# Kernel optimization log

Hardware: AMD Instinct MI355X
Metric: run time of the kernel (lower is better)

## Reference

```python
import jax, jax.numpy as jnp
import numpy as np

B, N, CIN, COUT = 4, 4096, 64, 64

def setup_inputs() -> dict:
    key = jax.random.key(0)
    k1, k2, k3, k4, k5 = jax.random.split(key, 5)
    X = jax.random.normal(k1, (B, N, CIN), dtype=jnp.float32)
    A = jax.random.uniform(k2, (N, N), dtype=jnp.float32)
    weight1 = jax.random.normal(k3, (CIN, COUT), dtype=jnp.float32) * 0.05
    weight2 = jax.random.normal(k4, (1 * COUT, COUT), dtype=jnp.float32) * 0.05
    alpha = jax.random.normal(k5, (2 * COUT, 1), dtype=jnp.float32) * 0.05
    return {"X": X, "A": A, "weight1": weight1, "weight2": weight2, "alpha": alpha}

def reference(X, A, weight1, weight2, alpha):
    n = A.shape[0]
    c = weight1.shape[1]
    b = X.shape[0]
    # add self loops on the adjacency diagonal
    idx = jnp.arange(n)
    adj = A.at[idx, idx].set(1.0)
    # node transform: [B,N,C]
    out = jnp.matmul(X, weight1)
    # edge feature (P=1): [N,N,1], row-normalized over j (axis=1)
    E = adj[:, :, None]
    E_wave = E / E.sum(axis=1, keepdims=True)
    # attention scores via rank-1 decomposition of alpha
    att_l = jnp.matmul(out, alpha[:c])   # [B,N,1]
    att_r = jnp.matmul(out, alpha[c:])   # [B,N,1]
    scores = jax.nn.leaky_relu(att_l @ jnp.swapaxes(att_r, 1, 2))  # [B,N,N]
    # exp + edge-feature weighting: [P,B,N,N]
    att = jnp.einsum('bij,ijp->pbij', jnp.exp(scores), E_wave)
    # manual softmax-style normalization over neighbors j
    att = att / att.sum(axis=-1, keepdims=True)
    # aggregate: [B,N,P,C] -> [B,N,P*C]
    agg = jnp.einsum('pbij,bjc->bipc', att, out).reshape(b, n, -1)
    return jnp.matmul(agg, weight2)
```

## Files before the change

### kernel.cpp

```cpp
#include <hip/hip_runtime.h>
#include <hip/hip_bf16.h>

typedef __attribute__((ext_vector_type(8))) short short8;
typedef __attribute__((ext_vector_type(4))) float floatx4;
typedef unsigned int u32;

#define NN 4096

static __device__ __forceinline__ unsigned f2bf_rne(float x) {
    union { float f; unsigned u; } v; v.f = x;
    unsigned r = v.u + 0x7fffu + ((v.u >> 16) & 1u);
    return r >> 16;
}
static __device__ __forceinline__ float bf2f(unsigned hi) {
    union { unsigned u; float f; } v; v.u = hi << 16; return v.f;
}

static __device__ __forceinline__ void gld16(void* l, const void* g) {
    __builtin_amdgcn_global_load_lds(
        (const __attribute__((address_space(1))) u32*)g,
        (__attribute__((address_space(3))) u32*)l, 16, 0, 0);
}

__global__ __launch_bounds__(256, 1)
void wc_kernel(const float* __restrict__ W1,
               const float* __restrict__ W2,
               const float* __restrict__ alpha,
               float* __restrict__ WcstG,
               float* __restrict__ w1aG) {
    __shared__ __align__(16) float W1s[64 * 68];
    __shared__ __align__(16) float W2s[64 * 68];
    __shared__ float als[128];
    const int t = threadIdx.x;
    #pragma unroll
    for (int s = 0; s < 4; ++s) {
        int idx = s * 1024 + t * 4;
        int r = idx >> 6, cc = idx & 63;
        *(float4*)&W1s[r * 68 + cc] = *(const float4*)(W1 + idx);
        *(float4*)&W2s[r * 68 + cc] = *(const float4*)(W2 + idx);
    }
    if (t < 128) als[t] = alpha[t];
    __syncthreads();
    const int k = t >> 2, nq = t & 3;
    float acc[16];
    #pragma unroll
    for (int i = 0; i < 16; ++i) acc[i] = 0.f;
    for (int mm = 0; mm < 64; ++mm) {
        float w1v = W1s[k * 68 + mm];
        #pragma unroll
        for (int i = 0; i < 16; ++i)
            acc[i] += w1v * W2s[mm * 68 + nq * 16 + i];
    }
    #pragma unroll
    for (int i = 0; i < 16; ++i)
        WcstG[(nq * 16 + i) * 68 + k] = acc[i];
    if (t < 64) {
        float sl = 0.f, sr = 0.f;
        for (int cc2 = 0; cc2 < 64; ++cc2) {
            float wv = W1s[t * 68 + cc2];
            sl += wv * als[cc2];
            sr += wv * als[64 + cc2];
        }
        w1aG[t] = sl; w1aG[64 + t] = sr;
    }
}

__global__ __launch_bounds__(256, 4)
void prep_kernel(const float* __restrict__ X,
                 const float* __restrict__ WcstG,
                 const float* __restrict__ w1aG,
                 unsigned short* __restrict__ Gt,
                 float* __restrict__ lv,
                 float* __restrict__ rv) {
    __shared__ __align__(16) char sm[17920];
    float* Wcst = (float*)sm;
    float* w1s  = (float*)(sm + 17408);
    float* GsT  = (float*)sm;

    const int t = threadIdx.x;
    const int row0 = blockIdx.x * 64;
    const int b = row0 >> 12, n0 = row0 & (NN - 1);
    const int w = t >> 6, lane = t & 63;
    const int m = lane & 15, q = lane >> 4;

    const int row = row0 + w * 16 + m;
    const float* xp = X + (size_t)row * 64;
    float4 x0 = *(const float4*)(xp + q * 8);
    float4 x1 = *(const float4*)(xp + q * 8 + 4);
    float4 x2 = *(const float4*)(xp + 32 + q * 8);
    float4 x3 = *(const float4*)(xp + 32 + q * 8 + 4);

    #pragma unroll
    for (int it = 0; it < 5; ++it) {
        int i = it * 1024 + t * 4;
        if (i < 4352) *(float4*)&Wcst[i] = *(const float4*)(WcstG + i);
    }
    if (t < 128) w1s[t] = w1aG[t];
    __syncthreads();

    const float xs[16] = {x0.x,x0.y,x0.z,x0.w, x1.x,x1.y,x1.z,x1.w,
                          x2.x,x2.y,x2.z,x2.w, x3.x,x3.y,x3.z,x3.w};

    float pl = 0.f, pr = 0.f;
    #pragma unroll
    for (int ks = 0; ks < 2; ++ks)
        #pragma unroll
        for (int j = 0; j < 8; ++j) {
            int k = ks * 32 + q * 8 + j;
            float xv = xs[ks * 8 + j];
            pl += xv * w1s[k];
            pr += xv * w1s[64 + k];
        }
    pl += __shfl_xor(pl, 16, 64); pl += __shfl_xor(pl, 32, 64);
    pr += __shfl_xor(pr, 16, 64); pr += __shfl_xor(pr, 32, 64);
    if (q == 0) { lv[row] = pl; rv[row] = pr; }

    short8 ah[2], al[2];
    #pragma unroll
    for (int ks = 0; ks < 2; ++ks)
        #pragma unroll
        for (int j = 0; j < 8; ++j) {
            float f = xs[ks * 8 + j];
            unsigned hb = f2bf_rne(f);
            float res = f - bf2f(hb);
            ah[ks][j] = (short)hb;
            al[ks][j] = (short)f2bf_rne(res);
        }

    short8 bfr[4][2];
    #pragma unroll
    for (int nt = 0; nt < 4; ++nt)
        #pragma unroll
        for (int ks = 0; ks < 2; ++ks) {
            const float* wp = &Wcst[(nt * 16 + m) * 68 + ks * 32 + q * 8];
            float4 w0 = *(const float4*)wp;
            float4 w1 = *(const float4*)(wp + 4);
            short8 bf;
            bf[0] = (short)f2bf_rne(w0.x); bf[1] = (short)f2bf_rne(w0.y);
            bf[2] = (short)f2bf_rne(w0.z); bf[3] = (short)f2bf_rne(w0.w);
            bf[4] = (short)f2bf_rne(w1.x); bf[5] = (short)f2bf_rne(w1.y);
            bf[6] = (short)f2bf_rne(w1.z); bf[7] = (short)f2bf_rne(w1.w);
            bfr[nt][ks] = bf;
        }

    floatx4 acc[4] = {{0,0,0,0},{0,0,0,0},{0,0,0,0},{0,0,0,0}};
    #pragma unroll
    for (int ks = 0; ks < 2; ++ks)
        #pragma unroll
        for (int nt = 0; nt < 4; ++nt) {
            acc[nt] = __builtin_amdgcn_mfma_f32_16x16x32_bf16(ah[ks], bfr[nt][ks], acc[nt], 0, 0, 0);
            acc[nt] = __builtin_amdgcn_mfma_f32_16x16x32_bf16(al[ks], bfr[nt][ks], acc[nt], 0, 0, 0);
        }

    __syncthreads();
    #pragma unroll
    for (int nt = 0; nt < 4; ++nt)
        #pragma unroll
        for (int rg = 0; rg < 4; ++rg)
            GsT[(nt * 16 + m) * 68 + w * 16 + q * 4 + rg] = acc[nt][rg];
    __syncthreads();
    unsigned* Gu = (unsigned*)Gt;
    #pragma unroll
    for (int it2 = 0; it2 < 8; ++it2) {
        int c2 = (t >> 5) + it2 * 8;
        int np = t & 31;
        unsigned lo = f2bf_rne(GsT[c2 * 68 + 2 * np]);
        unsigned hi = f2bf_rne(GsT[c2 * 68 + 2 * np + 1]);
        Gu[(((((size_t)(b * 64 + c2)) << 12) + n0) >> 1) + np] = lo | (hi << 16);
    }
}

__global__ __launch_bounds__(1024, 4)
void attn_kernel(const float* __restrict__ A,
                 const unsigned short* __restrict__ Gt,
                 const float* __restrict__ lv,
                 const float* __restrict__ rv,
                 float* __restrict__ out) {
    __shared__ __align__(16) char sm[65536];

    const int bx = blockIdx.x;
    const int i0 = (bx & 63) * 64;
    const int b  = bx >> 6;
    const int t = threadIdx.x;
    const int wave = t >> 6, lane = t & 63;
    const int grp = wave >> 2, wsub = wave & 3;
    const int m = lane & 15, q = lane >> 4;
    const int irow = wsub * 16 + m;

    const float* aRow = A + (size_t)(i0 + irow) * NN + grp * 1024 + q * 8;
    const unsigned short* gRow = Gt + (((size_t)(b * 64 + irow)) << 12) + grp * 1024 + q * 8;
    const float* rvg = rv + (size_t)b * NN + grp * 1024 + q * 8;
    char* gdst = sm + grp * 4096 + wsub * 1024;

    const float li = lv[b * NN + i0 + irow] * 1.44269504f;
    const float li001 = li * 0.01f;

    gld16(gdst, gRow);
    float4 a0 = *(const float4*)(aRow);
    float4 a1 = *(const float4*)(aRow + 4);
    float4 r0 = *(const float4*)(rvg);
    float4 r1 = *(const float4*)(rvg + 4);

    const bool diag_grp = ((i0 >> 10) == grp);
    const int jd = (i0 + irow) - grp * 1024;

    floatx4 acc0 = {0,0,0,0}, acc1 = {0,0,0,0}, acc2 = {0,0,0,0}, acc3 = {0,0,0,0};
    float dsum = 0.f;

    unsigned short* Gbuf = (unsigned short*)sm;

    #pragma unroll 4
    for (int cc = 0; cc < 32; ++cc) {
        if (cc < 31) gld16(gdst + ((cc + 1) & 3) * 16384, gRow + (cc + 1) * 32);

        float aa[8] = {a0.x, a0.y, a0.z, a0.w, a1.x, a1.y, a1.z, a1.w};
        if (diag_grp && ((jd >> 5) == cc)) {
            const int dd = jd - (cc * 32 + q * 8);
            #pragma unroll
            for (int e = 0; e < 8; ++e) if (dd == e) aa[e] = 1.0f;
        }
        const float rr[8] = {r0.x, r0.y, r0.z, r0.w, r1.x, r1.y, r1.z, r1.w};
        unsigned up[8];
        #pragma unroll
        for (int e = 0; e < 8; ++e) {
            float s = fmaxf(li * rr[e], li001 * rr[e]);
            float ev = __builtin_amdgcn_exp2f(s) * aa[e];
            unsigned u = __float_as_uint(ev) + 0x8000u;
            up[e] = u;
            dsum += __uint_as_float(u & 0xffff0000u);
        }
        union { unsigned u[4]; short8 s8; } cv;
        cv.u[0] = __builtin_amdgcn_perm(up[1], up[0], 0x07060302u);
        cv.u[1] = __builtin_amdgcn_perm(up[3], up[2], 0x07060302u);
        cv.u[2] = __builtin_amdgcn_perm(up[5], up[4], 0x07060302u);
        cv.u[3] = __builtin_amdgcn_perm(up[7], up[6], 0x07060302u);
        const short8 afr = cv.s8;

        { const int jn = (cc < 31) ? (cc + 1) * 32 : 0;
          a0 = *(const float4*)(aRow + jn);
          a1 = *(const float4*)(aRow + jn + 4);
          r0 = *(const float4*)(rvg + jn);
          r1 = *(const float4*)(rvg + jn + 4); }

        __syncthreads();
        {
            const unsigned short* Gb = Gbuf + (cc & 3) * 8192 + grp * 2048;
            const short8 b0 = *(const short8*)&Gb[lane * 8];
            const short8 b1 = *(const short8*)&Gb[512 + lane * 8];
            const short8 b2 = *(const short8*)&Gb[1024 + lane * 8];
            const short8 b3 = *(const short8*)&Gb[1536 + lane * 8];
            acc0 = __builtin_amdgcn_mfma_f32_16x16x32_bf16(afr, b0, acc0, 0, 0, 0);
            acc1 = __builtin_amdgcn_mfma_f32_16x16x32_bf16(afr, b1, acc1, 0, 0, 0);
            acc2 = __builtin_amdgcn_mfma_f32_16x16x32_bf16(afr, b2, acc2, 0, 0, 0);
            acc3 = __builtin_amdgcn_mfma_f32_16x16x32_bf16(afr, b3, acc3, 0, 0, 0);
        }
    }

    dsum += __shfl_xor(dsum, 16, 64);
    dsum += __shfl_xor(dsum, 32, 64);

    __syncthreads();
    float* red = (float*)sm;
    const int il = t >> 4, c4 = t & 15;
    float4 osum = {0.f, 0.f, 0.f, 0.f};
    float dtot = 0.f;
    #pragma unroll
    for (int pass = 0; pass < 2; ++pass) {
        if ((grp >> 1) == pass) {
            float* rp_ = red + (grp & 1) * 4352;
            #pragma unroll
            for (int nt = 0; nt < 4; ++nt) {
                floatx4 av = nt == 0 ? acc0 : nt == 1 ? acc1 : nt == 2 ? acc2 : acc3;
                #pragma unroll
                for (int rg = 0; rg < 4; ++rg)
                    rp_[(wsub * 16 + q * 4 + rg) * 68 + nt * 16 + m] = av[rg];
            }
            if (q == 0) rp_[(wsub * 16 + m) * 68 + 64] = dsum;
        }
        __syncthreads();
        {
            float4 v0 = *(const float4*)&red[il * 68 + c4 * 4];
            float4 v1 = *(const float4*)&red[4352 + il * 68 + c4 * 4];
            osum.x += v0.x + v1.x; osum.y += v0.y + v1.y;
            osum.z += v0.z + v1.z; osum.w += v0.w + v1.w;
            dtot += red[il * 68 + 64] + red[4352 + il * 68 + 64];
        }
        __syncthreads();
    }
    const float rinv = 1.0f / dtot;
    float4 o;
    o.x = osum.x * rinv; o.y = osum.y * rinv;
    o.z = osum.z * rinv; o.w = osum.w * rinv;
    *(float4*)(out + (((size_t)(b * NN + i0 + il)) << 6) + c4 * 4) = o;
}

extern "C" void kernel_launch(void* const* d_in, const int* in_sizes, int n_in,
                              void* d_out, int out_size, void* d_ws, size_t ws_size,
                              hipStream_t stream) {
    const float* X     = (const float*)d_in[0];
    const float* A     = (const float*)d_in[1];
    const float* W1    = (const float*)d_in[2];
    const float* W2    = (const float*)d_in[3];
    const float* alpha = (const float*)d_in[4];
    float* out = (float*)d_out;

    char* ws = (char*)d_ws;
    unsigned short* Gt = (unsigned short*)(ws);
    float* lvp   = (float*)(ws + 2097152);
    float* rvp   = (float*)(ws + 2097152 + 65536);
    float* WcstG = (float*)(ws + 2097152 + 131072);
    float* w1aG  = (float*)(ws + 2097152 + 131072 + 17408);

    wc_kernel<<<1, 256, 0, stream>>>(W1, W2, alpha, WcstG, w1aG);
    prep_kernel<<<256, 256, 0, stream>>>(X, WcstG, w1aG, Gt, lvp, rvp);
    attn_kernel<<<256, 1024, 0, stream>>>(A, Gt, lvp, rvp, out);
}
```

Before: 175.1 us.

## Load G operands directly into registers with double buffering, drop LDS staging

The attention kernel now loads the bf16 G tiles for the MFMA B operand straight from global memory into registers, instead of staging them through LDS with global_load_lds and a per-iteration barrier. The main loop is unrolled by two with A-chunk and B-chunk register double buffering, and rv is cached once in shared memory. Dropping the per-chunk __syncthreads and shrinking LDS use is meant to cut synchronisation stalls. The cost is that each wave now reads G itself instead of sharing one staged copy, which raises redundant global and L2 traffic and register pressure.

```diff
diff --git a/kernel.cpp b/kernel.cpp
--- a/kernel.cpp
+++ b/kernel.cpp
@@ -14,12 +14,6 @@
 }
 static __device__ __forceinline__ float bf2f(unsigned hi) {
     union { unsigned u; float f; } v; v.u = hi << 16; return v.f;
-}
-
-static __device__ __forceinline__ void gld16(void* l, const void* g) {
-    __builtin_amdgcn_global_load_lds(
-        (const __attribute__((address_space(1))) u32*)g,
-        (__attribute__((address_space(3))) u32*)l, 16, 0, 0);
 }
 
 __global__ __launch_bounds__(256, 1)
@@ -176,7 +170,8 @@
                  const float* __restrict__ lv,
                  const float* __restrict__ rv,
                  float* __restrict__ out) {
-    __shared__ __align__(16) char sm[65536];
+    __shared__ __align__(16) char sm[34816];
+    float* rs = (float*)sm;
 
     const int bx = blockIdx.x;
     const int i0 = (bx & 63) * 64;
@@ -187,19 +182,29 @@
     const int m = lane & 15, q = lane >> 4;
     const int irow = wsub * 16 + m;
 
+    *(float4*)&rs[t * 4] = *(const float4*)(rv + (size_t)b * NN + t * 4);
+
     const float* aRow = A + (size_t)(i0 + irow) * NN + grp * 1024 + q * 8;
-    const unsigned short* gRow = Gt + (((size_t)(b * 64 + irow)) << 12) + grp * 1024 + q * 8;
-    const float* rvg = rv + (size_t)b * NN + grp * 1024 + q * 8;
-    char* gdst = sm + grp * 4096 + wsub * 1024;
+    const unsigned short* gB0 = Gt + (((size_t)(b * 64 + m)) << 12) + grp * 1024 + q * 8;
+    const unsigned short* gB1 = gB0 + ((size_t)16 << 12);
+    const unsigned short* gB2 = gB0 + ((size_t)32 << 12);
+    const unsigned short* gB3 = gB0 + ((size_t)48 << 12);
 
     const float li = lv[b * NN + i0 + irow] * 1.44269504f;
     const float li001 = li * 0.01f;
 
-    gld16(gdst, gRow);
-    float4 a0 = *(const float4*)(aRow);
-    float4 a1 = *(const float4*)(aRow + 4);
-    float4 r0 = *(const float4*)(rvg);
-    float4 r1 = *(const float4*)(rvg + 4);
+    float4 a0A = *(const float4*)(aRow);
+    float4 a1A = *(const float4*)(aRow + 4);
+    short8 b0A = *(const short8*)(gB0);
+    short8 b1A = *(const short8*)(gB1);
+    short8 b2A = *(const short8*)(gB2);
+    short8 b3A = *(const short8*)(gB3);
+    float4 a0B = *(const float4*)(aRow + 32);
+    float4 a1B = *(const float4*)(aRow + 36);
+    short8 b0B = *(const short8*)(gB0 + 32);
+    short8 b1B = *(const short8*)(gB1 + 32);
+    short8 b2B = *(const short8*)(gB2 + 32);
+    short8 b3B = *(const short8*)(gB3 + 32);
 
     const bool diag_grp = ((i0 >> 10) == grp);
     const int jd = (i0 + irow) - grp * 1024;
@@ -207,18 +212,17 @@
     floatx4 acc0 = {0,0,0,0}, acc1 = {0,0,0,0}, acc2 = {0,0,0,0}, acc3 = {0,0,0,0};
     float dsum = 0.f;
 
-    unsigned short* Gbuf = (unsigned short*)sm;
-
-    #pragma unroll 4
-    for (int cc = 0; cc < 32; ++cc) {
-        if (cc < 31) gld16(gdst + ((cc + 1) & 3) * 16384, gRow + (cc + 1) * 32);
-
+    __syncthreads();
+
+    auto genE = [&](float4 a0, float4 a1, int chunk) -> short8 {
         float aa[8] = {a0.x, a0.y, a0.z, a0.w, a1.x, a1.y, a1.z, a1.w};
-        if (diag_grp && ((jd >> 5) == cc)) {
-            const int dd = jd - (cc * 32 + q * 8);
+        if (diag_grp && ((jd >> 5) == chunk)) {
+            const int dd = jd - (chunk * 32 + q * 8);
             #pragma unroll
             for (int e = 0; e < 8; ++e) if (dd == e) aa[e] = 1.0f;
         }
+        const float4 r0 = *(const float4*)&rs[grp * 1024 + chunk * 32 + q * 8];
+        const float4 r1 = *(const float4*)&rs[grp * 1024 + chunk * 32 + q * 8 + 4];
         const float rr[8] = {r0.x, r0.y, r0.z, r0.w, r1.x, r1.y, r1.z, r1.w};
         unsigned up[8];
         #pragma unroll
@@ -234,25 +238,38 @@
         cv.u[1] = __builtin_amdgcn_perm(up[3], up[2], 0x07060302u);
         cv.u[2] = __builtin_amdgcn_perm(up[5], up[4], 0x07060302u);
         cv.u[3] = __builtin_amdgcn_perm(up[7], up[6], 0x07060302u);
-        const short8 afr = cv.s8;
-
-        { const int jn = (cc < 31) ? (cc + 1) * 32 : 0;
-          a0 = *(const float4*)(aRow + jn);
-          a1 = *(const float4*)(aRow + jn + 4);
-          r0 = *(const float4*)(rvg + jn);
-          r1 = *(const float4*)(rvg + jn + 4); }
-
-        __syncthreads();
+        return cv.s8;
+    };
+
+    #pragma unroll 2
+    for (int cc = 0; cc < 32; cc += 2) {
         {
-            const unsigned short* Gb = Gbuf + (cc & 3) * 8192 + grp * 2048;
-            const short8 b0 = *(const short8*)&Gb[lane * 8];
-            const short8 b1 = *(const short8*)&Gb[512 + lane * 8];
-            const short8 b2 = *(const short8*)&Gb[1024 + lane * 8];
-            const short8 b3 = *(const short8*)&Gb[1536 + lane * 8];
-            acc0 = __builtin_amdgcn_mfma_f32_16x16x32_bf16(afr, b0, acc0, 0, 0, 0);
-            acc1 = __builtin_amdgcn_mfma_f32_16x16x32_bf16(afr, b1, acc1, 0, 0, 0);
-            acc2 = __builtin_amdgcn_mfma_f32_16x16x32_bf16(afr, b2, acc2, 0, 0, 0);
-            acc3 = __builtin_amdgcn_mfma_f32_16x16x32_bf16(afr, b3, acc3, 0, 0, 0);
+            const short8 afr = genE(a0A, a1A, cc);
+            acc0 = __builtin_amdgcn_mfma_f32_16x16x32_bf16(afr, b0A, acc0, 0, 0, 0);
+            acc1 = __builtin_amdgcn_mfma_f32_16x16x32_bf16(afr, b1A, acc1, 0, 0, 0);
+            acc2 = __builtin_amdgcn_mfma_f32_16x16x32_bf16(afr, b2A, acc2, 0, 0, 0);
+            acc3 = __builtin_amdgcn_mfma_f32_16x16x32_bf16(afr, b3A, acc3, 0, 0, 0);
+            const int jn = (cc + 2 < 32) ? (cc + 2) * 32 : cc * 32;
+            a0A = *(const float4*)(aRow + jn);
+            a1A = *(const float4*)(aRow + jn + 4);
+            b0A = *(const short8*)(gB0 + jn);
+            b1A = *(const short8*)(gB1 + jn);
+            b2A = *(const short8*)(gB2 + jn);
+            b3A = *(const short8*)(gB3 + jn);
+        }
+        {
+            const short8 afr = genE(a0B, a1B, cc + 1);
+            acc0 = __builtin_amdgcn_mfma_f32_16x16x32_bf16(afr, b0B, acc0, 0, 0, 0);
+            acc1 = __builtin_amdgcn_mfma_f32_16x16x32_bf16(afr, b1B, acc1, 0, 0, 0);
+            acc2 = __builtin_amdgcn_mfma_f32_16x16x32_bf16(afr, b2B, acc2, 0, 0, 0);
+            acc3 = __builtin_amdgcn_mfma_f32_16x16x32_bf16(afr, b3B, acc3, 0, 0, 0);
+            const int jn = (cc + 3 < 32) ? (cc + 3) * 32 : (cc + 1) * 32;
+            a0B = *(const float4*)(aRow + jn);
+            a1B = *(const float4*)(aRow + jn + 4);
+            b0B = *(const short8*)(gB0 + jn);
+            b1B = *(const short8*)(gB1 + jn);
+            b2B = *(const short8*)(gB2 + jn);
+            b3B = *(const short8*)(gB3 + jn);
         }
     }
 
```

After: 198.4 us. 1.13x slower.

## Fuse weight precompute into prep kernel and rework attn G staging pipeline

Applied to the files above, without the earlier changes.

The tiny single-block wc_kernel is removed. Every prep block now recomputes W1·W2 and W1·alpha in shared memory, which drops a launch and a global round trip at the cost of redundant per-block work. In attn_kernel, the async global_load_lds quad-buffered G staging is replaced with register-staged loads written into a padded triple-buffered LDS ring. The main loop is unrolled by two with separate even/odd prefetch registers for A and rv, and uses a raw s_barrier with lgkmcnt wait. This is meant to hide the load latency of A and G and to cut LDS bank conflicts, but it costs more registers.

```diff
diff --git a/kernel.cpp b/kernel.cpp
--- a/kernel.cpp
+++ b/kernel.cpp
@@ -16,22 +16,35 @@
     union { unsigned u; float f; } v; v.u = hi << 16; return v.f;
 }
 
-static __device__ __forceinline__ void gld16(void* l, const void* g) {
-    __builtin_amdgcn_global_load_lds(
-        (const __attribute__((address_space(1))) u32*)g,
-        (__attribute__((address_space(3))) u32*)l, 16, 0, 0);
-}
-
-__global__ __launch_bounds__(256, 1)
-void wc_kernel(const float* __restrict__ W1,
-               const float* __restrict__ W2,
-               const float* __restrict__ alpha,
-               float* __restrict__ WcstG,
-               float* __restrict__ w1aG) {
-    __shared__ __align__(16) float W1s[64 * 68];
-    __shared__ __align__(16) float W2s[64 * 68];
-    __shared__ float als[128];
+__global__ __launch_bounds__(256, 4)
+void prep_kernel(const float* __restrict__ X,
+                 const float* __restrict__ W1,
+                 const float* __restrict__ W2,
+                 const float* __restrict__ alpha,
+                 unsigned short* __restrict__ Gt,
+                 float* __restrict__ lv,
+                 float* __restrict__ rv) {
+    __shared__ __align__(16) char sm[53248];
+    float* W1s  = (float*)sm;
+    float* W2s  = (float*)(sm + 17408);
+    float* Wcst = (float*)(sm + 34816);
+    float* w1s  = (float*)(sm + 52224);
+    float* als  = (float*)(sm + 52736);
+    float* GsT  = (float*)sm;
+
     const int t = threadIdx.x;
+    const int row0 = blockIdx.x * 64;
+    const int b = row0 >> 12, n0 = row0 & (NN - 1);
+    const int w = t >> 6, lane = t & 63;
+    const int m = lane & 15, q = lane >> 4;
+
+    const int row = row0 + w * 16 + m;
+    const float* xp = X + (size_t)row * 64;
+    float4 x0 = *(const float4*)(xp + q * 8);
+    float4 x1 = *(const float4*)(xp + q * 8 + 4);
+    float4 x2 = *(const float4*)(xp + 32 + q * 8);
+    float4 x3 = *(const float4*)(xp + 32 + q * 8 + 4);
+
     #pragma unroll
     for (int s = 0; s < 4; ++s) {
         int idx = s * 1024 + t * 4;
@@ -41,19 +54,22 @@
     }
     if (t < 128) als[t] = alpha[t];
     __syncthreads();
-    const int k = t >> 2, nq = t & 3;
-    float acc[16];
-    #pragma unroll
-    for (int i = 0; i < 16; ++i) acc[i] = 0.f;
-    for (int mm = 0; mm < 64; ++mm) {
-        float w1v = W1s[k * 68 + mm];
+
+    {
+        const int k = t >> 2, nq = t & 3;
+        float acc[16];
+        #pragma unroll
+        for (int i = 0; i < 16; ++i) acc[i] = 0.f;
+        for (int mm = 0; mm < 64; ++mm) {
+            float w1v = W1s[k * 68 + mm];
+            #pragma unroll
+            for (int i = 0; i < 16; ++i)
+                acc[i] += w1v * W2s[mm * 68 + nq * 16 + i];
+        }
         #pragma unroll
         for (int i = 0; i < 16; ++i)
-            acc[i] += w1v * W2s[mm * 68 + nq * 16 + i];
-    }
-    #pragma unroll
-    for (int i = 0; i < 16; ++i)
-        WcstG[(nq * 16 + i) * 68 + k] = acc[i];
+            Wcst[(nq * 16 + i) * 68 + k] = acc[i];
+    }
     if (t < 64) {
         float sl = 0.f, sr = 0.f;
         for (int cc2 = 0; cc2 < 64; ++cc2) {
@@ -61,41 +77,8 @@
             sl += wv * als[cc2];
             sr += wv * als[64 + cc2];
         }
-        w1aG[t] = sl; w1aG[64 + t] = sr;
-    }
-}
-
-__global__ __launch_bounds__(256, 4)
-void prep_kernel(const float* __restrict__ X,
-                 const float* __restrict__ WcstG,
-                 const float* __restrict__ w1aG,
-                 unsigned short* __restrict__ Gt,
-                 float* __restrict__ lv,
-                 float* __restrict__ rv) {
-    __shared__ __align__(16) char sm[17920];
-    float* Wcst = (float*)sm;
-    float* w1s  = (float*)(sm + 17408);
-    float* GsT  = (float*)sm;
-
-    const int t = threadIdx.x;
-    const int row0 = blockIdx.x * 64;
-    const int b = row0 >> 12, n0 = row0 & (NN - 1);
-    const int w = t >> 6, lane = t & 63;
-    const int m = lane & 15, q = lane >> 4;
-
-    const int row = row0 + w * 16 + m;
-    const float* xp = X + (size_t)row * 64;
-    float4 x0 = *(const float4*)(xp + q * 8);
-    float4 x1 = *(const float4*)(xp + q * 8 + 4);
-    float4 x2 = *(const float4*)(xp + 32 + q * 8);
-    float4 x3 = *(const float4*)(xp + 32 + q * 8 + 4);
-
-    #pragma unroll
-    for (int it = 0; it < 5; ++it) {
-        int i = it * 1024 + t * 4;
-        if (i < 4352) *(float4*)&Wcst[i] = *(const float4*)(WcstG + i);
-    }
-    if (t < 128) w1s[t] = w1aG[t];
+        w1s[t] = sl; w1s[64 + t] = sr;
+    }
     __syncthreads();
 
     const float xs[16] = {x0.x,x0.y,x0.z,x0.w, x1.x,x1.y,x1.z,x1.w,
@@ -176,7 +159,8 @@
                  const float* __restrict__ lv,
                  const float* __restrict__ rv,
                  float* __restrict__ out) {
-    __shared__ __align__(16) char sm[65536];
+    __shared__ __align__(16) char sm[61440];
+    unsigned short* Gs = (unsigned short*)sm;
 
     const int bx = blockIdx.x;
     const int i0 = (bx & 63) * 64;
@@ -185,37 +169,44 @@
     const int wave = t >> 6, lane = t & 63;
     const int grp = wave >> 2, wsub = wave & 3;
     const int m = lane & 15, q = lane >> 4;
-    const int irow = wsub * 16 + m;
-
-    const float* aRow = A + (size_t)(i0 + irow) * NN + grp * 1024 + q * 8;
-    const unsigned short* gRow = Gt + (((size_t)(b * 64 + irow)) << 12) + grp * 1024 + q * 8;
-    const float* rvg = rv + (size_t)b * NN + grp * 1024 + q * 8;
-    char* gdst = sm + grp * 4096 + wsub * 1024;
-
-    const float li = lv[b * NN + i0 + irow] * 1.44269504f;
+    const int irE = wsub * 16 + m;
+    const int irS = wsub * 16 + (lane >> 2);
+    const int jseg = lane & 3;
+
+    const float* aRow = A + (size_t)(i0 + irE) * NN + grp * 1024 + q * 8;
+    const float* rvp  = rv + (size_t)b * NN + grp * 1024 + q * 8;
+    const unsigned short* gRow = Gt + (((size_t)(b * 64 + irS)) << 12) + grp * 1024 + jseg * 8;
+
+    const float li = lv[b * NN + i0 + irE] * 1.44269504f;
     const float li001 = li * 0.01f;
-
-    gld16(gdst, gRow);
-    float4 a0 = *(const float4*)(aRow);
-    float4 a1 = *(const float4*)(aRow + 4);
-    float4 r0 = *(const float4*)(rvg);
-    float4 r1 = *(const float4*)(rvg + 4);
-
     const bool diag_grp = ((i0 >> 10) == grp);
-    const int jd = (i0 + irow) - grp * 1024;
+    const int jd = (i0 + irE) - grp * 1024;
+
+    const int soff = irS * 40 + jseg * 8;
+    unsigned short* GsG = Gs + grp * 2560;
+
+    short8 sg = *(const short8*)(gRow);
+    float4 a0E = *(const float4*)(aRow);
+    float4 a1E = *(const float4*)(aRow + 4);
+    float4 r0E = *(const float4*)(rvp);
+    float4 r1E = *(const float4*)(rvp + 4);
+    float4 a0O = *(const float4*)(aRow + 32);
+    float4 a1O = *(const float4*)(aRow + 36);
+    float4 r0O = *(const float4*)(rvp + 32);
+    float4 r1O = *(const float4*)(rvp + 36);
+    *(short8*)&GsG[soff] = sg;
+    sg = *(const short8*)(gRow + 32);
+    asm volatile("s_waitcnt lgkmcnt(0)" ::: "memory");
+    __builtin_amdgcn_s_barrier();
+    __builtin_amdgcn_sched_barrier(0);
 
     floatx4 acc0 = {0,0,0,0}, acc1 = {0,0,0,0}, acc2 = {0,0,0,0}, acc3 = {0,0,0,0};
     float dsum = 0.f;
 
-    unsigned short* Gbuf = (unsigned short*)sm;
-
-    #pragma unroll 4
-    for (int cc = 0; cc < 32; ++cc) {
-        if (cc < 31) gld16(gdst + ((cc + 1) & 3) * 16384, gRow + (cc + 1) * 32);
-
+    auto genE = [&](float4 a0, float4 a1, float4 r0, float4 r1, int chunk) -> short8 {
         float aa[8] = {a0.x, a0.y, a0.z, a0.w, a1.x, a1.y, a1.z, a1.w};
-        if (diag_grp && ((jd >> 5) == cc)) {
-            const int dd = jd - (cc * 32 + q * 8);
+        if (diag_grp && ((jd >> 5) == chunk)) {
+            const int dd = jd - (chunk * 32 + q * 8);
             #pragma unroll
             for (int e = 0; e < 8; ++e) if (dd == e) aa[e] = 1.0f;
         }
@@ -234,25 +225,55 @@
         cv.u[1] = __builtin_amdgcn_perm(up[3], up[2], 0x07060302u);
         cv.u[2] = __builtin_amdgcn_perm(up[5], up[4], 0x07060302u);
         cv.u[3] = __builtin_amdgcn_perm(up[7], up[6], 0x07060302u);
-        const short8 afr = cv.s8;
-
-        { const int jn = (cc < 31) ? (cc + 1) * 32 : 0;
-          a0 = *(const float4*)(aRow + jn);
-          a1 = *(const float4*)(aRow + jn + 4);
-          r0 = *(const float4*)(rvg + jn);
-          r1 = *(const float4*)(rvg + jn + 4); }
-
-        __syncthreads();
+        return cv.s8;
+    };
+
+    for (int cc = 0; cc < 32; cc += 2) {
         {
-            const unsigned short* Gb = Gbuf + (cc & 3) * 8192 + grp * 2048;
-            const short8 b0 = *(const short8*)&Gb[lane * 8];
-            const short8 b1 = *(const short8*)&Gb[512 + lane * 8];
-            const short8 b2 = *(const short8*)&Gb[1024 + lane * 8];
-            const short8 b3 = *(const short8*)&Gb[1536 + lane * 8];
+            *(short8*)&GsG[((cc + 1) % 3) * 10240 + soff] = sg;
+            { const int jn = (cc + 2 < 32) ? (cc + 2) * 32 : 0;
+              sg = *(const short8*)(gRow + jn); }
+            const short8 afr = genE(a0E, a1E, r0E, r1E, cc);
+            { const int jn = (cc + 2 < 32) ? (cc + 2) * 32 : 0;
+              a0E = *(const float4*)(aRow + jn);
+              a1E = *(const float4*)(aRow + jn + 4);
+              r0E = *(const float4*)(rvp + jn);
+              r1E = *(const float4*)(rvp + jn + 4); }
+            const unsigned short* rb = &GsG[(cc % 3) * 10240];
+            const short8 b0 = *(const short8*)&rb[( m) * 40 + q * 8];
+            const short8 b1 = *(const short8*)&rb[(16 + m) * 40 + q * 8];
+            const short8 b2 = *(const short8*)&rb[(32 + m) * 40 + q * 8];
+            const short8 b3 = *(const short8*)&rb[(48 + m) * 40 + q * 8];
             acc0 = __builtin_amdgcn_mfma_f32_16x16x32_bf16(afr, b0, acc0, 0, 0, 0);
             acc1 = __builtin_amdgcn_mfma_f32_16x16x32_bf16(afr, b1, acc1, 0, 0, 0);
             acc2 = __builtin_amdgcn_mfma_f32_16x16x32_bf16(afr, b2, acc2, 0, 0, 0);
             acc3 = __builtin_amdgcn_mfma_f32_16x16x32_bf16(afr, b3, acc3, 0, 0, 0);
+            asm volatile("s_waitcnt lgkmcnt(0)" ::: "memory");
+            __builtin_amdgcn_s_barrier();
+            __builtin_amdgcn_sched_barrier(0);
+        }
+        {
+            *(short8*)&GsG[((cc + 2) % 3) * 10240 + soff] = sg;
+            { const int jn = (cc + 3 < 32) ? (cc + 3) * 32 : 0;
+              sg = *(const short8*)(gRow + jn); }
+            const short8 afr = genE(a0O, a1O, r0O, r1O, cc + 1);
+            { const int jn = (cc + 3 < 32) ? (cc + 3) * 32 : 0;
+              a0O = *(const float4*)(aRow + jn);
+              a1O = *(const float4*)(aRow + jn + 4);
+              r0O = *(const float4*)(rvp + jn);
+              r1O = *(const float4*)(rvp + jn + 4); }
+            const unsigned short* rb = &GsG[((cc + 1) % 3) * 10240];
+            const short8 b0 = *(const short8*)&rb[( m) * 40 + q * 8];
+            const short8 b1 = *(const short8*)&rb[(16 + m) * 40 + q * 8];
+            const short8 b2 = *(const short8*)&rb[(32 + m) * 40 + q * 8];
+            const short8 b3 = *(const short8*)&rb[(48 + m) * 40 + q * 8];
+            acc0 = __builtin_amdgcn_mfma_f32_16x16x32_bf16(afr, b0, acc0, 0, 0, 0);
+            acc1 = __builtin_amdgcn_mfma_f32_16x16x32_bf16(afr, b1, acc1, 0, 0, 0);
+            acc2 = __builtin_amdgcn_mfma_f32_16x16x32_bf16(afr, b2, acc2, 0, 0, 0);
+            acc3 = __builtin_amdgcn_mfma_f32_16x16x32_bf16(afr, b3, acc3, 0, 0, 0);
+            asm volatile("s_waitcnt lgkmcnt(0)" ::: "memory");
+            __builtin_amdgcn_s_barrier();
+            __builtin_amdgcn_sched_barrier(0);
         }
     }
 
@@ -306,12 +327,9 @@
 
     char* ws = (char*)d_ws;
     unsigned short* Gt = (unsigned short*)(ws);
-    float* lvp   = (float*)(ws + 2097152);
-    float* rvp   = (float*)(ws + 2097152 + 65536);
-    float* WcstG = (float*)(ws + 2097152 + 131072);
-    float* w1aG  = (float*)(ws + 2097152 + 131072 + 17408);
-
-    wc_kernel<<<1, 256, 0, stream>>>(W1, W2, alpha, WcstG, w1aG);
-    prep_kernel<<<256, 256, 0, stream>>>(X, WcstG, w1aG, Gt, lvp, rvp);
+    float* lvp = (float*)(ws + 2097152);
+    float* rvp = (float*)(ws + 2097152 + 65536);
+
+    prep_kernel<<<256, 256, 0, stream>>>(X, W1, W2, alpha, Gt, lvp, rvp);
     attn_kernel<<<256, 1024, 0, stream>>>(A, Gt, lvp, rvp, out);
 }
```

Result: faster. 157.1 us (-10.2%).
